# Kernel optimization log

Measured on AMD Instinct MI355X. Metric: run time of the kernel, lower is better.

## Reference

```python
import jax, jax.numpy as jnp
import numpy as np

H = 200  # hidden size
D = 1    # input size
T = 8192 # sequence length


def setup_inputs() -> dict:
    key = jax.random.key(0)
    ks = jax.random.split(key, 11)
    s = 1.0 / np.sqrt(H)  # torch LSTM init scale
    u = lambda k, shape: jax.random.uniform(k, shape, jnp.float32, -s, s)
    return {
        "input_seq": jax.random.normal(ks[0], (T, D), jnp.float32),
        "W_ih0": u(ks[1], (4 * H, D)),
        "W_hh0": u(ks[2], (4 * H, H)),
        "b_ih0": u(ks[3], (4 * H,)),
        "b_hh0": u(ks[4], (4 * H,)),
        "W_ih1": u(ks[5], (4 * H, H)),
        "W_hh1": u(ks[6], (4 * H, H)),
        "b_ih1": u(ks[7], (4 * H,)),
        "b_hh1": u(ks[8], (4 * H,)),
        "W_out": u(ks[9], (D, H)),
        "b_out": u(ks[10], (D,)),
    }


def _cell(pre, h, c, Whh):
    # pre: [4H] = x @ W_ih.T + b_ih + b_hh already folded in
    g = pre + h @ Whh.T
    i, f, gg, o = jnp.split(g, 4)
    i = jax.nn.sigmoid(i)
    f = jax.nn.sigmoid(f)
    gg = jnp.tanh(gg)
    o = jax.nn.sigmoid(o)
    c = f * c + i * gg
    h = o * jnp.tanh(c)
    return h, c


def reference(input_seq, W_ih0, W_hh0, b_ih0, b_hh0,
              W_ih1, W_hh1, b_ih1, b_hh1, W_out, b_out):
    x = input_seq.reshape(input_seq.shape[0], -1)  # [T, D]
    # precompute layer-0 input projections for all timesteps (one big GEMM)
    pre0 = x @ W_ih0.T + (b_ih0 + b_hh0)           # [T, 4H]
    b1 = b_ih1 + b_hh1

    def step(carry, p0):
        h0, c0, h1, c1 = carry
        h0, c0 = _cell(p0, h0, c0, W_hh0)
        # eval mode: dropout(0.1) between layers is identity
        h1, c1 = _cell(h0 @ W_ih1.T + b1, h1, c1, W_hh1)
        return (h0, c0, h1, c1), None

    z = jnp.zeros((H,), x.dtype)
    (h0, c0, h1, c1), _ = jax.lax.scan(step, (z, z, z, z), pre0)
    # predictions[-1]: linear head on last top-layer hidden state -> [D]
    return h1 @ W_out.T + b_out
```

## Files before the change

kernel.cpp:

```cpp
#include <hip/hip_runtime.h>

#define TT 8192
#define HH 200
#define G4 800
#define NLJ 9
#define NWR 64
#define RD 1024
#define RDM 1023
#define BPWIN 900

typedef unsigned long long u64;
typedef unsigned int u32;
typedef _Float16 f16;
typedef _Float16 f16x2 __attribute__((ext_vector_type(2)));

__device__ __forceinline__ float sigmoidf_(float x){ return 1.0f/(1.0f+__expf(-x)); }
__device__ __forceinline__ float tanhf_(float x){
    float e = __expf(2.0f*fabsf(x));
    float r = 1.0f - 2.0f/(e + 1.0f);
    return copysignf(r, x);
}
__device__ __forceinline__ u64 pcku(u32 tag, u32 v){ return ((u64)tag<<32) | v; }
__device__ __forceinline__ u64 pckf(u32 tag, float v){ return pcku(tag, __float_as_uint(v)); }
__device__ __forceinline__ u64 ald(const u64* p){
    return __hip_atomic_load((u64*)p, __ATOMIC_RELAXED, __HIP_MEMORY_SCOPE_AGENT);
}
__device__ __forceinline__ void ast(u64* p, u64 v){
    __hip_atomic_store(p, v, __ATOMIC_RELAXED, __HIP_MEMORY_SCOPE_AGENT);
}
__device__ __forceinline__ u32 pkh(float a, float b){
    f16x2 v = { (f16)a, (f16)b };
    return __builtin_bit_cast(u32, v);
}
__device__ __forceinline__ float dot2(u32 a, u32 b, float c){
#if __has_builtin(__builtin_amdgcn_fdot2)
    return __builtin_amdgcn_fdot2(__builtin_bit_cast(f16x2, a),
                                  __builtin_bit_cast(f16x2, b), c, false);
#else
    f16x2 av = __builtin_bit_cast(f16x2, a), bv = __builtin_bit_cast(f16x2, b);
    return c + (float)av[0]*(float)bv[0] + (float)av[1]*(float)bv[1];
#endif
}
__device__ __forceinline__ u32 poll1u(const u64* p, u32 tag){
    u64 v; do { v = ald(p); } while ((u32)(v >> 32) != tag);
    return (u32)v;
}
__device__ __forceinline__ void poll5(const u64* slot, u32 tag, int m, float* o){
    const bool g4 = (m < 32);
    u64 v0, v1, v2, v3, v4 = 0;
    for(;;){
        v0 = ald(slot + m);       v1 = ald(slot + m + 192);
        v2 = ald(slot + m + 384); v3 = ald(slot + m + 576);
        if (g4) v4 = ald(slot + m + 768);
        if ((u32)(v0>>32)==tag && (u32)(v1>>32)==tag && (u32)(v2>>32)==tag &&
            (u32)(v3>>32)==tag && (!g4 || (u32)(v4>>32)==tag)) break;
    }
    o[0]=__uint_as_float((u32)v0); o[1]=__uint_as_float((u32)v1);
    o[2]=__uint_as_float((u32)v2); o[3]=__uint_as_float((u32)v3);
    o[4]= g4 ? __uint_as_float((u32)v4) : 0.f;
}

__global__ __launch_bounds__(1024, 4)
void lstm_pipe(const float* __restrict__ x,
               const float* __restrict__ Wih0, const float* __restrict__ Whh0,
               const float* __restrict__ bih0, const float* __restrict__ bhh0,
               const float* __restrict__ Wih1, const float* __restrict__ Whh1,
               const float* __restrict__ bih1, const float* __restrict__ bhh1,
               const float* __restrict__ Wout, const float* __restrict__ bout,
               u64* __restrict__ hp0,
               u64* __restrict__ p1r,
               u32* __restrict__ prog,
               float* __restrict__ out)
{
    const int role = blockIdx.x;
    const int tid  = threadIdx.x;

    __shared__ __align__(16) u32 wl[NLJ * G4 * 4];
    __shared__ __align__(16) u32 hp_lds[100];
    __shared__ float h32[HH];
    __shared__ float s_pre[G4];
    __shared__ float xr[8];
    __shared__ u32 hpbuf[2][100];

    if (role >= 2) {
        const int q = role - 2;
        const int rl = tid >> 2, kq = tid & 3;
        u32 wp[25]; float bs = 0.f; int grow = 0;
        if (tid < 800) {
            grow = q * 200 + rl;
            const float* wr = Wih1 + (size_t)grow * HH + kq * 50;
            #pragma unroll
            for (int i = 0; i < 25; ++i) wp[i] = pkh(wr[2*i], wr[2*i+1]);
            #pragma unroll
            for (int i = 0; i < 25; ++i) asm volatile("" : "+v"(wp[i]));
            if (kq == 0) bs = bih1[grow] + bhh1[grow];
        } else if (tid >= 832 && tid < 932) {
            hpbuf[0][tid - 832] = poll1u(&hp0[tid - 832], 1u);
        }
        u32 prog_c = 0;
        __syncthreads();
        for (int t = 0; t < TT; ++t) {
            if (tid < 800) {
                const u32* hb = hpbuf[t & 1] + kq * 25;
                float a0 = 0.f, a1 = 0.f;
                #pragma unroll
                for (int i = 0; i < 25; i += 2) a0 = dot2(wp[i], hb[i], a0);
                #pragma unroll
                for (int i = 1; i < 25; i += 2) a1 = dot2(wp[i], hb[i], a1);
                float s = a0 + a1;
                s += __shfl_xor(s, 1);
                s += __shfl_xor(s, 2);
                if (kq == 0)
                    ast(&p1r[(size_t)(t & RDM) * G4 + grow],
                        pckf((u32)(t + 1), s + bs));
            } else if (tid >= 832 && tid < 932) {
                if (t + 1 < TT)
                    hpbuf[(t + 1) & 1][tid - 832] =
                        poll1u(&hp0[(size_t)(t + 1) * 100 + (tid - 832)],
                               (u32)(t + 2));
            } else if (tid == 1008) {
                while ((int)(t + 1) - (int)prog_c >= BPWIN) {
                    __builtin_amdgcn_s_sleep(8);
                    prog_c = __hip_atomic_load(prog, __ATOMIC_RELAXED,
                                               __HIP_MEMORY_SCOPE_AGENT);
                }
            }
            __syncthreads();
        }
        return;
    }

    const bool L0 = (role == 0);
    const float* Whh = L0 ? Whh0 : Whh1;

    for (int idx = tid; idx < G4 * 36; idx += 1024) {
        const int r = idx / 36, p = idx % 36;
        const float* wr = Whh + (size_t)r * HH;
        wl[(((p >> 2) * G4 + r) << 2) + (p & 3)] = pkh(wr[2*p], wr[2*p + 1]);
    }
    u32 w[NWR]; float wih = 0.f, bs = 0.f;
    if (tid < G4) {
        const float* wr = Whh + (size_t)tid * HH + 72;
        #pragma unroll
        for (int i = 0; i < NWR; ++i) w[i] = pkh(wr[2*i], wr[2*i + 1]);
        #pragma unroll
        for (int i = 0; i < NWR; ++i) asm volatile("" : "+v"(w[i]));
        if (L0) {
            bs = bih0[tid] + bhh0[tid];
            wih = Wih0[tid];
            asm volatile("" : "+v"(bs));
            asm volatile("" : "+v"(wih));
        }
    }
    if (tid < 100) hp_lds[tid] = 0u;
    if (tid < HH) h32[tid] = 0.f;

    float c = 0.f, c2 = 0.f;
    float o0=0.f, o1=0.f, o2=0.f, o3=0.f, o4=0.f;
    if (!L0 && tid >= 832) {
        float o[5];
        poll5(p1r, 1u, tid - 832, o);
        const int m = tid - 832;
        s_pre[m] = o[0]; s_pre[m+192] = o[1]; s_pre[m+384] = o[2];
        s_pre[m+576] = o[3];
        if (m < 32) s_pre[m+768] = o[4];
    }
    if (L0 && tid == 832) xr[0] = x[0];
    __syncthreads();

    for (int t = 0; t < TT; ++t) {
        if (tid < G4) {
            const uint4* hp4 = (const uint4*)hp_lds;
            float a0=0.f, a1=0.f, a2=0.f, a3=0.f;
            #pragma unroll
            for (int j = 0; j < NLJ; ++j) {
                const uint4 hu = hp4[j];
                const uint4 wu = *(const uint4*)&wl[(j * G4 + tid) << 2];
                a0 = dot2(wu.x, hu.x, a0);
                a1 = dot2(wu.y, hu.y, a1);
                a2 = dot2(wu.z, hu.z, a2);
                a3 = dot2(wu.w, hu.w, a3);
                if ((j % 3) == 2) __builtin_amdgcn_sched_barrier(0);
            }
            #pragma unroll
            for (int j = NLJ; j < 25; ++j) {
                const uint4 hu = hp4[j];
                const int i = (j - NLJ) * 4;
                a0 = dot2(w[i],     hu.x, a0);
                a1 = dot2(w[i + 1], hu.y, a1);
                a2 = dot2(w[i + 2], hu.z, a2);
                a3 = dot2(w[i + 3], hu.w, a3);
                if ((j % 4) == 3) __builtin_amdgcn_sched_barrier(0);
            }
            const float acc = (a0 + a1) + (a2 + a3);
            if (L0) s_pre[tid] = acc + xr[t & 7] * wih + bs;
            else    s_pre[tid] = acc + s_pre[tid];
        } else if (tid >= 832) {
            if (!L0) {
                if (t + 1 < TT) {
                    float o[5];
                    poll5(&p1r[(size_t)((t + 1) & RDM) * G4], (u32)(t + 2),
                          tid - 832, o);
                    o0=o[0]; o1=o[1]; o2=o[2]; o3=o[3]; o4=o[4];
                }
            } else if (tid == 832 && t + 1 < TT) {
                o0 = x[t + 1];
            }
        }
        __syncthreads();
        if (tid >= 832) {
            const int n = tid - 832;
            const float ig = sigmoidf_(s_pre[n]);
            const float fg = sigmoidf_(s_pre[200 + n]);
            const float gg = tanhf_  (s_pre[400 + n]);
            const float og = sigmoidf_(s_pre[600 + n]);
            c = fg * c + ig * gg;
            const float h = og * tanhf_(c);
            h32[n] = h;
            const float hpart = __shfl_xor(h, 1);
            u32 pk2 = 0;
            if (!(n & 1)) { pk2 = pkh(h, hpart); hp_lds[n >> 1] = pk2; }
            float h2 = 0.f;
            if (n < 8) {
                const int n2 = 192 + n;
                const float ig2 = sigmoidf_(s_pre[n2]);
                const float fg2 = sigmoidf_(s_pre[200 + n2]);
                const float gg2 = tanhf_  (s_pre[400 + n2]);
                const float og2 = sigmoidf_(s_pre[600 + n2]);
                c2 = fg2 * c2 + ig2 * gg2;
                h2 = og2 * tanhf_(c2);
                h32[n2] = h2;
            }
            const float h2part = __shfl_xor(h2, 1);
            u32 pk2b = 0;
            if (n < 8 && !(n & 1)) { pk2b = pkh(h2, h2part); hp_lds[96 + (n>>1)] = pk2b; }
            if (L0 && !(n & 1)) {
                ast(&hp0[(size_t)t * 100 + (n >> 1)], pcku((u32)(t + 1), pk2));
                if (n < 8)
                    ast(&hp0[(size_t)t * 100 + 96 + (n >> 1)],
                        pcku((u32)(t + 1), pk2b));
            }
        } else if (!L0 && tid == 800 && (t & 63) == 63) {
            __hip_atomic_store(prog, (u32)(t + 1), __ATOMIC_RELAXED,
                               __HIP_MEMORY_SCOPE_AGENT);
        }
        __syncthreads();
        if (tid >= 832 && t + 1 < TT) {
            if (!L0) {
                const int m = tid - 832;
                s_pre[m] = o0; s_pre[m+192] = o1; s_pre[m+384] = o2;
                s_pre[m+576] = o3;
                if (m < 32) s_pre[m+768] = o4;
            } else if (tid == 832) {
                xr[(t + 1) & 7] = o0;
            }
        }
        __syncthreads();
    }

    if (!L0 && tid < 64) {
        float s2 = 0.f;
        for (int k = tid; k < HH; k += 64) s2 += h32[k] * Wout[k];
        #pragma unroll
        for (int off = 32; off > 0; off >>= 1) s2 += __shfl_down(s2, off);
        if (tid == 0) out[0] = s2 + bout[0];
    }
}

extern "C" void kernel_launch(void* const* d_in, const int* in_sizes, int n_in,
                              void* d_out, int out_size, void* d_ws, size_t ws_size,
                              hipStream_t stream) {
    const float* x    = (const float*)d_in[0];
    const float* Wih0 = (const float*)d_in[1];
    const float* Whh0 = (const float*)d_in[2];
    const float* bih0 = (const float*)d_in[3];
    const float* bhh0 = (const float*)d_in[4];
    const float* Wih1 = (const float*)d_in[5];
    const float* Whh1 = (const float*)d_in[6];
    const float* bih1 = (const float*)d_in[7];
    const float* bhh1 = (const float*)d_in[8];
    const float* Wout = (const float*)d_in[9];
    const float* bout = (const float*)d_in[10];
    float* out = (float*)d_out;

    char* ws = (char*)d_ws;
    u64* hp0  = (u64*)ws;
    u64* p1r  = (u64*)(ws + 6553600);
    u32* prog = (u32*)(ws + 13107200);

    hipMemsetAsync(ws, 0, 13107264, stream);

    hipLaunchKernelGGL(lstm_pipe, dim3(6), dim3(1024), 0, stream,
        x, Wih0, Whh0, bih0, bhh0, Wih1, Whh1, bih1, bhh1, Wout, bout,
        hp0, p1r, prog, out);
}
```

Baseline: 16.02 ms.

## Double-buffer hidden state and input projections to drop a per-step barrier

Makes the packed hidden-state buffer and the layer-1 input-projection buffer double-buffered, indexed by step parity. This lets the gate-activation threads write next-step data directly, so the third __syncthreads per timestep can be removed from the serial recurrence loop. It also lowers the launch-bounds occupancy hint from 4 to 1. The cost is extra LDS and parity-indexed addressing. Correctness depends on the remaining two barriers ordering the buffer reuse properly.

```diff
diff --git a/kernel.cpp b/kernel.cpp
--- a/kernel.cpp
+++ b/kernel.cpp
@@ -60,7 +60,7 @@
     o[4]= g4 ? __uint_as_float((u32)v4) : 0.f;
 }
 
-__global__ __launch_bounds__(1024, 4)
+__global__ __launch_bounds__(1024, 1)
 void lstm_pipe(const float* __restrict__ x,
                const float* __restrict__ Wih0, const float* __restrict__ Whh0,
                const float* __restrict__ bih0, const float* __restrict__ bhh0,
@@ -76,10 +76,11 @@
     const int tid  = threadIdx.x;
 
     __shared__ __align__(16) u32 wl[NLJ * G4 * 4];
-    __shared__ __align__(16) u32 hp_lds[100];
+    __shared__ __align__(16) u32 hp_lds[2][100];
     __shared__ float h32[HH];
     __shared__ float s_pre[G4];
-    __shared__ float xr[8];
+    __shared__ float s_in[2][G4];
+    __shared__ float xr[2];
     __shared__ u32 hpbuf[2][100];
 
     if (role >= 2) {
@@ -152,7 +153,7 @@
             asm volatile("" : "+v"(wih));
         }
     }
-    if (tid < 100) hp_lds[tid] = 0u;
+    if (tid < 100) { hp_lds[0][tid] = 0u; hp_lds[1][tid] = 0u; }
     if (tid < HH) h32[tid] = 0.f;
 
     float c = 0.f, c2 = 0.f;
@@ -161,16 +162,17 @@
         float o[5];
         poll5(p1r, 1u, tid - 832, o);
         const int m = tid - 832;
-        s_pre[m] = o[0]; s_pre[m+192] = o[1]; s_pre[m+384] = o[2];
-        s_pre[m+576] = o[3];
-        if (m < 32) s_pre[m+768] = o[4];
+        s_in[0][m] = o[0]; s_in[0][m+192] = o[1]; s_in[0][m+384] = o[2];
+        s_in[0][m+576] = o[3];
+        if (m < 32) s_in[0][m+768] = o[4];
     }
     if (L0 && tid == 832) xr[0] = x[0];
     __syncthreads();
 
     for (int t = 0; t < TT; ++t) {
+        const int p = t & 1;
         if (tid < G4) {
-            const uint4* hp4 = (const uint4*)hp_lds;
+            const uint4* hp4 = (const uint4*)hp_lds[p];
             float a0=0.f, a1=0.f, a2=0.f, a3=0.f;
             #pragma unroll
             for (int j = 0; j < NLJ; ++j) {
@@ -193,8 +195,8 @@
                 if ((j % 4) == 3) __builtin_amdgcn_sched_barrier(0);
             }
             const float acc = (a0 + a1) + (a2 + a3);
-            if (L0) s_pre[tid] = acc + xr[t & 7] * wih + bs;
-            else    s_pre[tid] = acc + s_pre[tid];
+            if (L0) s_pre[tid] = acc + xr[p] * wih + bs;
+            else    s_pre[tid] = acc + s_in[p][tid];
         } else if (tid >= 832) {
             if (!L0) {
                 if (t + 1 < TT) {
@@ -219,7 +221,7 @@
             h32[n] = h;
             const float hpart = __shfl_xor(h, 1);
             u32 pk2 = 0;
-            if (!(n & 1)) { pk2 = pkh(h, hpart); hp_lds[n >> 1] = pk2; }
+            if (!(n & 1)) { pk2 = pkh(h, hpart); hp_lds[p ^ 1][n >> 1] = pk2; }
             float h2 = 0.f;
             if (n < 8) {
                 const int n2 = 192 + n;
@@ -233,27 +235,26 @@
             }
             const float h2part = __shfl_xor(h2, 1);
             u32 pk2b = 0;
-            if (n < 8 && !(n & 1)) { pk2b = pkh(h2, h2part); hp_lds[96 + (n>>1)] = pk2b; }
+            if (n < 8 && !(n & 1)) { pk2b = pkh(h2, h2part); hp_lds[p ^ 1][96 + (n>>1)] = pk2b; }
             if (L0 && !(n & 1)) {
                 ast(&hp0[(size_t)t * 100 + (n >> 1)], pcku((u32)(t + 1), pk2));
                 if (n < 8)
                     ast(&hp0[(size_t)t * 100 + 96 + (n >> 1)],
                         pcku((u32)(t + 1), pk2b));
             }
+            if (t + 1 < TT) {
+                if (!L0) {
+                    const int m = n;
+                    s_in[p ^ 1][m] = o0; s_in[p ^ 1][m + 192] = o1;
+                    s_in[p ^ 1][m + 384] = o2; s_in[p ^ 1][m + 576] = o3;
+                    if (m < 32) s_in[p ^ 1][m + 768] = o4;
+                } else if (tid == 832) {
+                    xr[p ^ 1] = o0;
+                }
+            }
         } else if (!L0 && tid == 800 && (t & 63) == 63) {
             __hip_atomic_store(prog, (u32)(t + 1), __ATOMIC_RELAXED,
                                __HIP_MEMORY_SCOPE_AGENT);
-        }
-        __syncthreads();
-        if (tid >= 832 && t + 1 < TT) {
-            if (!L0) {
-                const int m = tid - 832;
-                s_pre[m] = o0; s_pre[m+192] = o1; s_pre[m+384] = o2;
-                s_pre[m+576] = o3;
-                if (m < 32) s_pre[m+768] = o4;
-            } else if (tid == 832) {
-                xr[(t + 1) & 7] = o0;
-            }
         }
         __syncthreads();
     }
```

Measured after the change: 15.15 ms. -5.4%, faster.
